# Kernel optimization log

Hardware: AMD Instinct MI355X
Metric: run time of the kernel (lower is better)

The kernel has to match this reference:

```python
import jax, jax.numpy as jnp
import numpy as np
import math

EPS = 1e-5  # BatchNorm eps

def _bn(x, g, b):
    # eval-mode BatchNorm2d with fresh running stats (mean=0, var=1); x is NCHW
    s = g / jnp.sqrt(1.0 + EPS)
    return x * s[None, :, None, None] + b[None, :, None, None]

def _conv1x1(x, w, b):
    # x: (B,C,H,W), w: (O,C)
    return jnp.einsum('bchw,oc->bohw', x, w) + b[None, :, None, None]

def _selective_scan(xs, dts, A, Bs, Cs, D, delta_bias):
    # xs,dts: (B,K,D,L); A: (K,D,N); Bs,Cs: (B,K,N,L); D,delta_bias: (K,D)
    delta = jax.nn.softplus(dts + delta_bias[None, :, :, None])  # (B,K,D,L)
    d_t = jnp.moveaxis(delta, -1, 0)  # (L,B,K,D)
    u_t = jnp.moveaxis(xs, -1, 0)     # (L,B,K,D)
    B_t = jnp.moveaxis(Bs, -1, 0)     # (L,B,K,N)
    C_t = jnp.moveaxis(Cs, -1, 0)     # (L,B,K,N)

    def step(h, inp):
        d, u, b, c = inp
        dA = jnp.exp(d[..., None] * A)                       # (B,K,D,N)
        h = dA * h + (d * u)[..., None] * b[:, :, None, :]   # (B,K,D,N)
        y = jnp.einsum('bkdn,bkn->bkd', h, c)
        return h, y

    h0 = jnp.zeros(xs.shape[:3] + (A.shape[-1],), xs.dtype)
    _, ys = jax.lax.scan(step, h0, (d_t, u_t, B_t, C_t))
    y = jnp.moveaxis(ys, 0, -1)  # (B,K,D,L)
    return y + D[None, :, :, None] * xs

def _ssm(x, x_proj_w, dt_w, dt_b, A_logs, Ds):
    # x: (B,C,H,W); 4-directional VMamba SS2D core
    B, C, H, W = x.shape
    L = H * W
    K = 4
    N = A_logs.shape[-1]
    R = dt_w.shape[-1]
    x_hw = x.reshape(B, C, L)
    x_wh = jnp.transpose(x, (0, 1, 3, 2)).reshape(B, C, L)
    xs = jnp.stack([x_hw, x_wh, x_hw[..., ::-1], x_wh[..., ::-1]], axis=1)  # (B,K,C,L)
    x_dbl = jnp.einsum('bkdl,kcd->bkcl', xs, x_proj_w)
    dts = jnp.einsum('bkrl,kdr->bkdl', x_dbl[:, :, :R], dt_w)
    Bs = x_dbl[:, :, R:R + N]
    Cs = x_dbl[:, :, R + N:R + 2 * N]
    A = -jnp.exp(A_logs).reshape(K, C, N)
    out_y = _selective_scan(xs, dts, A, Bs, Cs, Ds.reshape(K, C), dt_b)  # (B,K,C,L)
    inv = out_y[:, 2:4, :, ::-1]

    def wh_to_hw(t):
        return jnp.transpose(t.reshape(B, C, W, H), (0, 1, 3, 2)).reshape(B, C, L)

    y = out_y[:, 0] + inv[:, 0] + wh_to_hw(out_y[:, 1]) + wh_to_hw(inv[:, 1])
    return jnp.transpose(y, (0, 2, 1))  # (B,L,C)

def _forward(x, qkv_w, proj_w, proj_b, dw_w, dw_b, bn1_g, bn1_b,
             ci_w1, ci_b1, ci_bn_g, ci_bn_b, ci_w2, ci_b2,
             si_w1, si_b1, si_bn_g, si_bn_b, si_w2, si_b2,
             x_proj_w, dt_w, dt_b, A_logs, Ds, H, W):
    B, L, C = x.shape
    v = x @ qkv_w.T                                           # (B,L,C)
    v_img = jnp.transpose(v, (0, 2, 1)).reshape(B, C, H, W)
    # SSM (attention-replacement) branch
    att = _ssm(v_img, x_proj_w, dt_w, dt_b, A_logs, Ds)       # (B,L,C)
    # depthwise conv branch
    conv_x = jax.lax.conv_general_dilated(
        v_img, dw_w, (1, 1), 'SAME', feature_group_count=C,
        dimension_numbers=('NCHW', 'OIHW', 'NCHW'))
    conv_x = jax.nn.gelu(_bn(conv_x + dw_b[None, :, None, None], bn1_g, bn1_b), approximate=False)
    # C-Map: channel interaction from conv branch
    pooled = jnp.mean(conv_x, axis=(2, 3), keepdims=True)     # (B,C,1,1)
    cm = jax.nn.gelu(_bn(_conv1x1(pooled, ci_w1, ci_b1), ci_bn_g, ci_bn_b), approximate=False)
    cm = _conv1x1(cm, ci_w2, ci_b2)                           # (B,C,1,1)
    channel_map = cm.reshape(B, 1, C)
    # S-Map: spatial interaction from ssm branch
    att_img = jnp.transpose(att, (0, 2, 1)).reshape(B, C, H, W)
    sm = jax.nn.gelu(_bn(_conv1x1(att_img, si_w1, si_b1), si_bn_g, si_bn_b), approximate=False)
    sm = _conv1x1(sm, si_w2, si_b2)                           # (B,1,H,W)
    # adaptive interaction
    att = att * jax.nn.sigmoid(channel_map)
    conv_x = jax.nn.sigmoid(sm) * conv_x
    conv_x = jnp.transpose(conv_x.reshape(B, C, L), (0, 2, 1))
    return (att + conv_x) @ proj_w.T + proj_b

def setup_inputs() -> dict:
    key = jax.random.key(0)
    ks = jax.random.split(key, 16)
    Bsz, H, W, C = 2, 64, 64, 96
    N, K = 16, 4
    R = math.ceil(C / 16)  # dt_rank = 6
    L = H * W
    rn = lambda k, s, sc: jax.random.normal(k, s, jnp.float32) * sc
    inp = {
        'x': rn(ks[0], (Bsz, L, C), 1.0),
        'H': H, 'W': W,
        'qkv_w': rn(ks[1], (C, C), C ** -0.5),
        'proj_w': rn(ks[2], (C, C), C ** -0.5),
        'proj_b': jnp.zeros((C,), jnp.float32),
        'dw_w': rn(ks[3], (C, 1, 3, 3), 0.2),
        'dw_b': jnp.zeros((C,), jnp.float32),
        'bn1_g': jnp.ones((C,), jnp.float32), 'bn1_b': jnp.zeros((C,), jnp.float32),
        'ci_w1': rn(ks[4], (C // 8, C), C ** -0.5), 'ci_b1': jnp.zeros((C // 8,), jnp.float32),
        'ci_bn_g': jnp.ones((C // 8,), jnp.float32), 'ci_bn_b': jnp.zeros((C // 8,), jnp.float32),
        'ci_w2': rn(ks[5], (C, C // 8), (C // 8) ** -0.5), 'ci_b2': jnp.zeros((C,), jnp.float32),
        'si_w1': rn(ks[6], (C // 16, C), C ** -0.5), 'si_b1': jnp.zeros((C // 16,), jnp.float32),
        'si_bn_g': jnp.ones((C // 16,), jnp.float32), 'si_bn_b': jnp.zeros((C // 16,), jnp.float32),
        'si_w2': rn(ks[7], (1, C // 16), (C // 16) ** -0.5), 'si_b2': jnp.zeros((1,), jnp.float32),
        'x_proj_w': rn(ks[8], (K, R + 2 * N, C), C ** -0.5),
        'dt_w': jax.random.uniform(ks[9], (K, C, R), jnp.float32, -(R ** -0.5), R ** -0.5),
    }
    dt = jnp.exp(jax.random.uniform(ks[10], (K, C)) * (math.log(0.1) - math.log(0.001)) + math.log(0.001))
    dt = jnp.clip(dt, 1e-4, None)
    inp['dt_b'] = dt + jnp.log(-jnp.expm1(-dt))  # inverse-softplus init
    inp['A_logs'] = jnp.log(jnp.tile(jnp.arange(1, N + 1, dtype=jnp.float32), (K * C, 1)))  # (K*C, N)
    inp['Ds'] = jnp.ones((K * C,), jnp.float32)
    return inp

def reference(x, H, W, qkv_w, proj_w, proj_b, dw_w, dw_b, bn1_g, bn1_b,
              ci_w1, ci_b1, ci_bn_g, ci_bn_b, ci_w2, ci_b2,
              si_w1, si_b1, si_bn_g, si_bn_b, si_w2, si_b2,
              x_proj_w, dt_w, dt_b, A_logs, Ds):
    return _forward(x, qkv_w, proj_w, proj_b, dw_w, dw_b, bn1_g, bn1_b,
                    ci_w1, ci_b1, ci_bn_g, ci_bn_b, ci_w2, ci_b2,
                    si_w1, si_b1, si_bn_g, si_bn_b, si_w2, si_b2,
                    x_proj_w, dt_w, dt_b, A_logs, Ds, H, W)
```

## Files before the change

kernel.cpp:

```cpp
#include <hip/hip_runtime.h>
#include <math.h>

#define BB 2
#define CC 96
#define LL 4096
#define KK 4
#define SS 128
#define CHL 32
#define XD 40
#define BNS 0.9999950000374997f

__device__ __forceinline__ float fsigmoid(float x){ return 1.f/(1.f+__expf(-x)); }
__device__ __forceinline__ float fgelu(float x){ return 0.5f*x*(1.f+erff(x*0.70710678118654752f)); }
__device__ __forceinline__ void pow_tree(float q, float* Q){
  float q2=q*q, q4=q2*q2, q8=q4*q4;
  Q[0]=q;      Q[1]=q2;     Q[2]=q2*q;   Q[3]=q4;
  Q[4]=q4*q;   Q[5]=q4*q2;  Q[6]=Q[5]*q; Q[7]=q8;
  Q[8]=q8*q;   Q[9]=q8*q2;  Q[10]=Q[9]*q;Q[11]=q8*q4;
  Q[12]=Q[11]*q; Q[13]=Q[11]*q2; Q[14]=Q[13]*q; Q[15]=q8*q8;
}

__global__ __launch_bounds__(512) void kQ(const float* __restrict__ x,
                                          const float* __restrict__ qkv_w,
                                          float* __restrict__ v_hw){
  __shared__ float xl[96*33];
  int bid = blockIdx.x;
  int b = bid >> 7;
  int l0 = (bid & 127) << 5;
  int tid = threadIdx.x;
  for (int idx = tid; idx < 32*96; idx += 512){
    int pos = idx/96, c = idx - pos*96;
    xl[c*33+pos] = x[((size_t)b*LL + l0 + pos)*CC + c];
  }
  __syncthreads();
  int wv = tid >> 6, lane = tid & 63, pos = lane & 31, ch = lane >> 5;
  int c0 = ch*48;
  int ob = __builtin_amdgcn_readfirstlane(wv*12);
  float acc[12];
#pragma unroll
  for (int j = 0; j < 12; ++j) acc[j] = 0.f;
  for (int i = 0; i < 48; ++i){
    int c = c0 + i;
    float xv = xl[c*33+pos];
#pragma unroll
    for (int j = 0; j < 12; ++j) acc[j] += xv * qkv_w[(ob+j)*96 + c];
  }
#pragma unroll
  for (int j = 0; j < 12; ++j) acc[j] += __shfl_xor(acc[j], 32);
  if (ch == 0){
#pragma unroll
    for (int j = 0; j < 12; ++j)
      v_hw[((size_t)b*CC + ob + j)*LL + l0 + pos] = acc[j];
  }
}

__global__ __launch_bounds__(256) void kT(const float* __restrict__ src,
                                          float* __restrict__ dst){
  __shared__ float t[64*65];
  int bid = blockIdx.x;
  size_t base = (size_t)bid * LL;
  int tid = threadIdx.x;
  for (int idx = tid; idx < 4096; idx += 256){
    int h = idx>>6, w = idx&63;
    t[w*65+h] = src[base+idx];
  }
  __syncthreads();
  for (int idx = tid; idx < 4096; idx += 256)
    dst[base+idx] = t[(idx>>6)*65 + (idx&63)];
}

__global__ __launch_bounds__(512) void kP(const float* __restrict__ v_hw,
                                          const float* __restrict__ v_wh,
                                          const float* __restrict__ xpw,
                                          float* __restrict__ xdbl){
  __shared__ float ul[96*33];
  __shared__ float ol[32*40];
  int bid = blockIdx.x;
  int tile = bid & 127; int bk = bid >> 7; int k = bk & 3; int b = bk >> 2;
  int l0 = tile << 5;
  int tid = threadIdx.x;
  const float* vs = (k & 1) ? v_wh : v_hw;
  bool fwd = (k < 2);
  for (int idx = tid; idx < 96*32; idx += 512){
    int c = idx >> 5, t = idx & 31;
    int srci = fwd ? (l0+t) : (LL-1-(l0+t));
    ul[c*33+t] = vs[((size_t)b*CC + c)*LL + srci];
  }
  if (tid < 32){ ol[tid*40+6] = 0.f; ol[tid*40+7] = 0.f; }
  __syncthreads();
  int wv = tid >> 6, lane = tid & 63, pos = lane & 31, ch = lane >> 5;
  int c0 = ch*48;
  int obase = __builtin_amdgcn_readfirstlane((wv < 6) ? wv*5 : 30 + (wv-6)*4);
  int ocnt  = (wv < 6) ? 5 : 4;
  const float* wk = xpw + k*38*96;
  float acc[5];
#pragma unroll
  for (int j = 0; j < 5; ++j) acc[j] = 0.f;
  for (int i = 0; i < 48; ++i){
    int c = c0 + i;
    float uv = ul[c*33+pos];
#pragma unroll
    for (int j = 0; j < 5; ++j)
      if (j < ocnt) acc[j] += uv * wk[(obase+j)*96 + c];
  }
#pragma unroll
  for (int j = 0; j < 5; ++j) acc[j] += __shfl_xor(acc[j], 32);
  if (ch == 0){
#pragma unroll
    for (int j = 0; j < 5; ++j){
      if (j < ocnt){
        int cc = obase + j;
        int off = (cc < 6) ? cc : cc+2;
        ol[pos*40 + off] = acc[j];
      }
    }
  }
  __syncthreads();
  size_t rec = (((size_t)b*KK + k)*LL + l0)*XD;
  for (int idx = tid; idx < 32*40; idx += 512)
    xdbl[rec + idx] = ol[idx];
}

__global__ __launch_bounds__(128) void kC(const float* __restrict__ v_hw,
                                          const float* __restrict__ v_wh,
                                          const float* __restrict__ xdbl,
                                          const float* __restrict__ dt_w,
                                          const float* __restrict__ dt_b,
                                          const float* __restrict__ dw_w,
                                          const float* __restrict__ dw_b,
                                          const float* __restrict__ bn_g,
                                          const float* __restrict__ bn_b,
                                          float* __restrict__ hend,
                                          float* __restrict__ Pbuf,
                                          float* __restrict__ convx,
                                          float* __restrict__ partial2){
  __shared__ float ul[96*33];
  __shared__ __align__(16) float xl[CHL*XD];
  __shared__ float pl[34*65];
  __shared__ float red[2];
  int tid = threadIdx.x;
  if (blockIdx.x < 1024){
    int bid = blockIdx.x;
    int s = bid & 127; int bk = bid >> 7; int k = bk & 3; int b = bk >> 2;
    const float* vs = (k & 1) ? v_wh : v_hw;
    bool fwd = (k < 2);
    size_t xbase = (((size_t)b*KK + k)*LL + s*CHL)*XD;
    const float4* xg = (const float4*)(xdbl + xbase);
    float4* xl4 = (float4*)xl;
    for (int idx = tid; idx < CHL*XD/4; idx += 128) xl4[idx] = xg[idx];
    for (int idx = tid; idx < 96*CHL; idx += 128){
      int cr = idx >> 5, t = idx & 31;
      int gt = s*CHL + t;
      int srci = fwd ? gt : (LL-1-gt);
      ul[cr*33+t] = vs[((size_t)b*CC + cr)*LL + srci];
    }
    int c = tid;
    float dtw[6], dtb = 0.f, h[16], sumd = 0.f;
    if (c < 96){
      int cb = k*96+c;
#pragma unroll
      for (int r = 0; r < 6; ++r) dtw[r] = dt_w[cb*6+r];
      dtb = dt_b[cb];
#pragma unroll
      for (int n = 0; n < 16; ++n) h[n] = 0.f;
    }
    __syncthreads();
    if (c < 96){
      for (int t = 0; t < CHL; ++t){
        const float* xr = xl + t*XD;
        float4 r03 = *(const float4*)xr;
        float2 r45 = *(const float2*)(xr+4);
        float draw = dtb + r03.x*dtw[0]+r03.y*dtw[1]+r03.z*dtw[2]
                         + r03.w*dtw[3]+r45.x*dtw[4]+r45.y*dtw[5];
        float e = __expf(draw);
        float delta = (draw > 20.f) ? draw : __logf(1.f+e);
        float qd = __builtin_amdgcn_rcpf(1.f+e);
        sumd += delta;
        float du = delta * ul[c*33+t];
        float4 b0 = *(const float4*)(xr+8),  b1 = *(const float4*)(xr+12),
               b2 = *(const float4*)(xr+16), b3 = *(const float4*)(xr+20);
        float Bv[16] = {b0.x,b0.y,b0.z,b0.w, b1.x,b1.y,b1.z,b1.w,
                        b2.x,b2.y,b2.z,b2.w, b3.x,b3.y,b3.z,b3.w};
        float Q[16]; pow_tree(qd, Q);
#pragma unroll
        for (int n = 0; n < 16; ++n) h[n] = h[n]*Q[n] + du*Bv[n];
      }
      float P[16]; pow_tree(__expf(-sumd), P);
      size_t obf = ((((size_t)b*KK+k)*SS + s)*96 + c)*16;
#pragma unroll
      for (int q = 0; q < 4; ++q){
        *(float4*)(hend + obf + q*4) = make_float4(h[q*4+0],h[q*4+1],h[q*4+2],h[q*4+3]);
        *(float4*)(Pbuf + obf + q*4) = make_float4(P[q*4+0],P[q*4+1],P[q*4+2],P[q*4+3]);
      }
    }
  } else {
    int cb = blockIdx.x - 1024;
    int plane = cb >> 1;
    int half = cb & 1;
    int c = plane % 96;
    int h0 = half*32;
    size_t base = (size_t)plane * LL;
    for (int idx = tid; idx < 34*64; idx += 128){
      int r = idx >> 6, w = idx & 63;
      int h = h0 - 1 + r;
      pl[r*65+w] = (h >= 0 && h < 64) ? v_hw[base + h*64 + w] : 0.f;
    }
    __syncthreads();
    float w9[9];
#pragma unroll
    for (int i = 0; i < 9; ++i) w9[i] = dw_w[c*9+i];
    float bias = dw_b[c], g = bn_g[c]*BNS, bb = bn_b[c];
    float lsum = 0.f;
    for (int idx = tid; idx < 2048; idx += 128){
      int hh = idx >> 6, w = idx & 63;
      float acc = bias;
#pragma unroll
      for (int i = 0; i < 3; ++i)
#pragma unroll
        for (int j = -1; j <= 1; ++j){
          int w2 = w + j;
          if (w2 >= 0 && w2 < 64) acc += pl[(hh+i)*65 + w2] * w9[i*3 + (j+1)];
        }
      float val = fgelu(acc*g + bb);
      convx[base + (h0+hh)*64 + w] = val;
      lsum += val;
    }
#pragma unroll
    for (int off = 32; off >= 1; off >>= 1) lsum += __shfl_down(lsum, off);
    if ((tid & 63) == 0) red[tid>>6] = lsum;
    __syncthreads();
    if (tid == 0) partial2[cb] = red[0] + red[1];
  }
}

__global__ __launch_bounds__(256) void kD(const float* __restrict__ hend,
                                          const float* __restrict__ Pbuf,
                                          float* __restrict__ Hin){
  int bid = blockIdx.x;
  int cpair = bid % 48; int bk = bid / 48;
  int tid = threadIdx.x;
  int sg = tid & 7;
  int n  = (tid >> 3) & 15;
  int c  = cpair*2 + (tid >> 7);
  int lane = tid & 63;
  size_t base = (size_t)bk*SS*1536 + c*16 + n;
  float he[16], pb[16];
  float A = 1.f, Bv = 0.f;
#pragma unroll
  for (int i = 0; i < 16; ++i){
    size_t off = base + (size_t)(sg*16+i)*1536;
    he[i] = hend[off]; pb[i] = Pbuf[off];
    A *= pb[i];
    Bv = he[i] + pb[i]*Bv;
  }
#pragma unroll
  for (int d = 1; d <= 4; d <<= 1){
    float Ap = __shfl(A, lane-d);
    float Bp = __shfl(Bv, lane-d);
    if (sg >= d){ Bv = A*Bp + Bv; A = A*Ap; }
  }
  float Bin = __shfl(Bv, lane-1);
  float hacc = (sg == 0) ? 0.f : Bin;
#pragma unroll
  for (int i = 0; i < 16; ++i){
    size_t off = base + (size_t)(sg*16+i)*1536;
    Hin[off] = hacc;
    hacc = he[i] + pb[i]*hacc;
  }
}

__global__ __launch_bounds__(128) void kE(const float* __restrict__ v_hw,
                                          const float* __restrict__ v_wh,
                                          const float* __restrict__ xdbl,
                                          const float* __restrict__ dt_w,
                                          const float* __restrict__ dt_b,
                                          const float* __restrict__ Hin,
                                          float* __restrict__ ybuf){
  __shared__ float ul[96*33];
  __shared__ float yl[96*33];
  __shared__ __align__(16) float xl[CHL*XD];
  int bid = blockIdx.x;
  int s = bid & 127; int bk = bid >> 7; int k = bk & 3; int b = bk >> 2;
  int tid = threadIdx.x;
  const float* vs = (k & 1) ? v_wh : v_hw;
  bool fwd = (k < 2);
  float* yo = ybuf + (size_t)k*786432;
  size_t xbase = (((size_t)b*KK + k)*LL + s*CHL)*XD;
  const float4* xg = (const float4*)(xdbl + xbase);
  float4* xl4 = (float4*)xl;
  for (int idx = tid; idx < CHL*XD/4; idx += 128) xl4[idx] = xg[idx];
  for (int idx = tid; idx < 96*CHL; idx += 128){
    int cr = idx >> 5, t = idx & 31;
    int gt = s*CHL + t;
    int srci = fwd ? gt : (LL-1-gt);
    ul[cr*33+t] = vs[((size_t)b*CC + cr)*LL + srci];
  }
  int c = tid;
  float dtw[6], dtb = 0.f, h[16];
  if (c < 96){
    int cb = k*96 + c;
#pragma unroll
    for (int r = 0; r < 6; ++r) dtw[r] = dt_w[cb*6+r];
    dtb = dt_b[cb];
    size_t hb = ((((size_t)b*KK+k)*SS + s)*96 + c)*16;
#pragma unroll
    for (int q = 0; q < 4; ++q){
      float4 hv = *(const float4*)(Hin + hb + q*4);
      h[q*4+0]=hv.x; h[q*4+1]=hv.y; h[q*4+2]=hv.z; h[q*4+3]=hv.w;
    }
  }
  __syncthreads();
  if (c < 96){
    for (int t = 0; t < CHL; ++t){
      const float* xr = xl + t*XD;
      float4 r03 = *(const float4*)xr;
      float2 r45 = *(const float2*)(xr+4);
      float draw = dtb + r03.x*dtw[0]+r03.y*dtw[1]+r03.z*dtw[2]
                       + r03.w*dtw[3]+r45.x*dtw[4]+r45.y*dtw[5];
      float e = __expf(draw);
      float delta = (draw > 20.f) ? draw : __logf(1.f+e);
      float qd = __builtin_amdgcn_rcpf(1.f+e);
      float du = delta * ul[c*33+t];
      float4 b0 = *(const float4*)(xr+8),  b1 = *(const float4*)(xr+12),
             b2 = *(const float4*)(xr+16), b3 = *(const float4*)(xr+20);
      float4 c0v = *(const float4*)(xr+24), c1v = *(const float4*)(xr+28),
             c2v = *(const float4*)(xr+32), c3v = *(const float4*)(xr+36);
      float Bv[16] = {b0.x,b0.y,b0.z,b0.w, b1.x,b1.y,b1.z,b1.w,
                      b2.x,b2.y,b2.z,b2.w, b3.x,b3.y,b3.z,b3.w};
      float Cv[16] = {c0v.x,c0v.y,c0v.z,c0v.w, c1v.x,c1v.y,c1v.z,c1v.w,
                      c2v.x,c2v.y,c2v.z,c2v.w, c3v.x,c3v.y,c3v.z,c3v.w};
      float Q[16]; pow_tree(qd, Q);
      float ya[4] = {0.f,0.f,0.f,0.f};
#pragma unroll
      for (int n = 0; n < 16; ++n){
        h[n] = h[n]*Q[n] + du*Bv[n];
        ya[n & 3] += h[n]*Cv[n];
      }
      yl[c*33+t] = (ya[0]+ya[1]) + (ya[2]+ya[3]);
    }
  }
  __syncthreads();
  for (int idx = tid; idx < 96*CHL; idx += 128){
    int cr = idx >> 5, t = idx & 31;
    int gt = s*CHL + t;
    int pos = fwd ? gt : (LL-1-gt);
    yo[((size_t)b*CC + cr)*LL + pos] = yl[cr*33+t];
  }
}

__global__ __launch_bounds__(256) void kF(const float* __restrict__ ybuf,
                                          const float* __restrict__ v_hw,
                                          const float* __restrict__ Ds,
                                          float* __restrict__ att){
  __shared__ float t1[64*65];
  int bid = blockIdx.x; int c = bid % 96;
  size_t base = (size_t)bid * LL;
  int tid = threadIdx.x;
  const float* yk0 = ybuf;
  const float* yk1 = ybuf + 786432;
  const float* yk2 = ybuf + 2*786432;
  const float* yk3 = ybuf + 3*786432;
  for (int idx = tid; idx < 4096; idx += 256)
    t1[(idx & 63)*65 + (idx >> 6)] = yk1[base+idx] + yk3[base+idx];
  __syncthreads();
  float dsum = Ds[c] + Ds[96+c] + Ds[192+c] + Ds[288+c];
  for (int idx = tid; idx < 4096; idx += 256){
    int h = idx >> 6, w = idx & 63;
    att[base+idx] = yk0[base+idx] + yk2[base+idx] + t1[h*65+w] + dsum*v_hw[base+idx];
  }
}

__global__ __launch_bounds__(512) void kG(const float* __restrict__ att,
                                          const float* __restrict__ convx,
                                          const float* __restrict__ partial2,
                                          const float* __restrict__ ci_w1, const float* __restrict__ ci_b1,
                                          const float* __restrict__ ci_g1, const float* __restrict__ ci_bb1,
                                          const float* __restrict__ ci_w2, const float* __restrict__ ci_b2,
                                          const float* __restrict__ si_w1, const float* __restrict__ si_b1,
                                          const float* __restrict__ si_g1, const float* __restrict__ si_bb1,
                                          const float* __restrict__ si_w2, const float* __restrict__ si_b2,
                                          const float* __restrict__ proj_w,
                                          const float* __restrict__ proj_b,
                                          float* __restrict__ out){
  __shared__ float ga[96*33];
  __shared__ float gc[96*33];
  __shared__ float pool[96];
  __shared__ float mid[12];
  __shared__ float smj[6*33];
  __shared__ float smv[32];
  __shared__ float cmv[96];
  int bid = blockIdx.x;
  int b = bid >> 7; int l0 = (bid & 127) << 5;
  int tid = threadIdx.x;
  for (int idx = tid; idx < 96*32; idx += 512){
    int c = idx >> 5, t = idx & 31;
    size_t gsrc = ((size_t)b*CC + c)*LL + l0 + t;
    ga[c*33+t] = att[gsrc];
    gc[c*33+t] = convx[gsrc];
  }
  if (tid < 96) pool[tid] = (partial2[(b*96+tid)*2] + partial2[(b*96+tid)*2+1]) * (1.f/4096.f);
  __syncthreads();
  int wv = tid >> 6, lane = tid & 63, pos = lane & 31, ch = lane >> 5;
  if (wv < 6){
    int j = __builtin_amdgcn_readfirstlane(wv);
    float dot = 0.f;
    for (int i = 0; i < 48; ++i){
      int c = ch*48 + i;
      dot += ga[c*33+pos] * si_w1[j*96+c];
    }
    dot += __shfl_xor(dot, 32);
    if (ch == 0)
      smj[j*33+pos] = si_w2[j]*fgelu((dot+si_b1[j])*si_g1[j]*BNS + si_bb1[j]);
  } else if (wv == 6 && lane < 12){
    int j2 = lane;
    float a = ci_b1[j2];
    for (int c = 0; c < 96; ++c) a += ci_w1[j2*96+c]*pool[c];
    mid[j2] = fgelu(a*ci_g1[j2]*BNS + ci_bb1[j2]);
  }
  __syncthreads();
  if (tid < 32){
    float sv = si_b2[0];
#pragma unroll
    for (int j = 0; j < 6; ++j) sv += smj[j*33+tid];
    smv[tid] = fsigmoid(sv);
  }
  if (tid >= 64 && tid < 160){
    int c = tid - 64;
    float a = ci_b2[c];
#pragma unroll
    for (int j = 0; j < 12; ++j) a += ci_w2[c*12+j]*mid[j];
    cmv[c] = fsigmoid(a);
  }
  __syncthreads();
  for (int idx = tid; idx < 96*32; idx += 512){
    int c = idx >> 5, t = idx & 31;
    ga[c*33+t] = ga[c*33+t]*cmv[c] + gc[c*33+t]*smv[t];
  }
  __syncthreads();
  int ob = __builtin_amdgcn_readfirstlane(wv*12);
  float acc[12];
#pragma unroll
  for (int j = 0; j < 12; ++j) acc[j] = 0.f;
  for (int i = 0; i < 48; ++i){
    int c = ch*48 + i;
    float gv = ga[c*33+pos];
#pragma unroll
    for (int j = 0; j < 12; ++j) acc[j] += gv * proj_w[(ob+j)*96 + c];
  }
#pragma unroll
  for (int j = 0; j < 12; ++j) acc[j] += __shfl_xor(acc[j], 32);
  if (ch == 0){
    float* ol = gc;
#pragma unroll
    for (int j = 0; j < 12; ++j) ol[pos*97 + ob + j] = acc[j] + proj_b[ob+j];
  }
  __syncthreads();
  const float* ol = gc;
  for (int idx = tid; idx < 32*96; idx += 512){
    int p = idx/96, o = idx - p*96;
    out[((size_t)b*LL + l0 + p)*CC + o] = ol[p*97+o];
  }
}

extern "C" void kernel_launch(void* const* d_in, const int* in_sizes, int n_in,
                              void* d_out, int out_size, void* d_ws, size_t ws_size,
                              hipStream_t stream) {
  const float* x      = (const float*)d_in[0];
  const float* qkv_w  = (const float*)d_in[3];
  const float* proj_w = (const float*)d_in[4];
  const float* proj_b = (const float*)d_in[5];
  const float* dw_w   = (const float*)d_in[6];
  const float* dw_b   = (const float*)d_in[7];
  const float* bn1_g  = (const float*)d_in[8];
  const float* bn1_b  = (const float*)d_in[9];
  const float* ci_w1  = (const float*)d_in[10];
  const float* ci_b1  = (const float*)d_in[11];
  const float* ci_bn_g= (const float*)d_in[12];
  const float* ci_bn_b= (const float*)d_in[13];
  const float* ci_w2  = (const float*)d_in[14];
  const float* ci_b2  = (const float*)d_in[15];
  const float* si_w1  = (const float*)d_in[16];
  const float* si_b1  = (const float*)d_in[17];
  const float* si_bn_g= (const float*)d_in[18];
  const float* si_bn_b= (const float*)d_in[19];
  const float* si_w2  = (const float*)d_in[20];
  const float* si_b2  = (const float*)d_in[21];
  const float* xpw    = (const float*)d_in[22];
  const float* dt_w   = (const float*)d_in[23];
  const float* dt_b   = (const float*)d_in[24];
  const float* Ds     = (const float*)d_in[26];

  float* ws    = (float*)d_ws;
  float* v_hw  = ws;
  float* v_wh  = v_hw + 786432;
  float* xdbl  = v_wh + 786432;
  float* hend  = xdbl + 1310720;
  float* Pbuf  = hend + 1572864;
  float* Hin   = Pbuf + 1572864;
  float* convx = Hin  + 1572864;
  float* partial2 = convx + 786432;
  float* ybuf  = hend;
  float* att   = xdbl;
  float* out = (float*)d_out;

  hipLaunchKernelGGL(kQ, dim3(256),  dim3(512), 0, stream, x, qkv_w, v_hw);
  hipLaunchKernelGGL(kT, dim3(192),  dim3(256), 0, stream, v_hw, v_wh);
  hipLaunchKernelGGL(kP, dim3(1024), dim3(512), 0, stream, v_hw, v_wh, xpw, xdbl);
  hipLaunchKernelGGL(kC, dim3(1408), dim3(128), 0, stream, v_hw, v_wh, xdbl, dt_w, dt_b,
                     dw_w, dw_b, bn1_g, bn1_b, hend, Pbuf, convx, partial2);
  hipLaunchKernelGGL(kD, dim3(384),  dim3(256), 0, stream, hend, Pbuf, Hin);
  hipLaunchKernelGGL(kE, dim3(1024), dim3(128), 0, stream, v_hw, v_wh, xdbl, dt_w, dt_b, Hin, ybuf);
  hipLaunchKernelGGL(kF, dim3(192),  dim3(256), 0, stream, ybuf, v_hw, Ds, att);
  hipLaunchKernelGGL(kG, dim3(256),  dim3(512), 0, stream, att, convx, partial2,
                     ci_w1, ci_b1, ci_bn_g, ci_bn_b, ci_w2, ci_b2,
                     si_w1, si_b1, si_bn_g, si_bn_b, si_w2, si_b2,
                     proj_w, proj_b, out);
}
```

Baseline: 217.5 us.

## Fuse all stages into one persistent cooperative kernel with grid syncs

Replaces the eight separate kernel launches with a single cooperative persistent kernel that runs each stage as a grid-strided phase separated by grid-wide syncs. A fallback path launches the phases as separate kernels. It also changes data layouts: qkv output is written both channel-last and planar, the transpose becomes a row copy in channel-last order, and the scans read u directly from global memory with a prefetch instead of staging it in shared memory. The aim is to remove launch gaps and tail effects between stages, at the cost of grid-sync overhead, a grid capped at 512 blocks, and lower occupancy from the shared-memory union.

```diff
diff --git a/kernel.cpp b/kernel.cpp
--- a/kernel.cpp
+++ b/kernel.cpp
@@ -1,5 +1,8 @@
 #include <hip/hip_runtime.h>
+#include <hip/hip_cooperative_groups.h>
 #include <math.h>
+
+namespace cg = cooperative_groups;
 
 #define BB 2
 #define CC 96
@@ -20,152 +23,186 @@
   Q[12]=Q[11]*q; Q[13]=Q[11]*q2; Q[14]=Q[13]*q; Q[15]=q8*q8;
 }
 
-__global__ __launch_bounds__(512) void kQ(const float* __restrict__ x,
-                                          const float* __restrict__ qkv_w,
-                                          float* __restrict__ v_hw){
-  __shared__ float xl[96*33];
-  int bid = blockIdx.x;
-  int b = bid >> 7;
-  int l0 = (bid & 127) << 5;
+struct Params {
+  const float *x,*qkv_w,*proj_w,*proj_b,*dw_w,*dw_b,*bn_g,*bn_b;
+  const float *ci_w1,*ci_b1,*ci_g1,*ci_bb1,*ci_w2,*ci_b2;
+  const float *si_w1,*si_b1,*si_g1,*si_bb1,*si_w2,*si_b2;
+  const float *xpw,*dt_w,*dt_b,*Ds;
+  float *vT_hw,*vP_hw,*vT_wh,*xdbl,*hend,*Pbuf,*Hin,*convxP,*partial,*ybuf,*out;
+};
+
+struct Ph1 { float xl[96*33]; };
+struct Ph2 { float t[64*65]; float red[4]; };
+struct Ph3 { float ul[96*33]; float ol[32*40]; };
+struct Ph4 { float xl[2][CHL*XD]; };
+struct Ph8 { float ga[96*33]; float gcv[96*33]; float pool[96]; float dsc[96];
+             float mid[12]; float smj[6*33]; float smv[32]; float cmv[96]; };
+union __align__(16) SMem { Ph1 p1; Ph2 p2; Ph3 p3; Ph4 p4; Ph8 p8; };
+
+__device__ void ph_qkv(SMem* sm, const Params& p){
+  int tid = threadIdx.x, wv = tid>>6, lane = tid&63;
+  int G = gridDim.x;
+  for (int it = blockIdx.x; it < 256; it += G){
+    int b = it >> 7, l0 = (it & 127) << 5;
+    __syncthreads();
+    const float* xs = p.x + ((size_t)b*LL + l0)*CC;
+    for (int idx = tid; idx < 3072; idx += 256){
+      int t = idx/96, c = idx - t*96;
+      sm->p1.xl[c*33+t] = xs[idx];
+    }
+    __syncthreads();
+    int pos = lane & 31, ch = lane >> 5, c0 = ch*48;
+    int ob = __builtin_amdgcn_readfirstlane(wv*24);
+    float acc[24];
+#pragma unroll
+    for (int j = 0; j < 24; ++j) acc[j] = 0.f;
+    for (int i = 0; i < 48; ++i){
+      int c = c0 + i;
+      float xv = sm->p1.xl[c*33+pos];
+#pragma unroll
+      for (int j = 0; j < 24; ++j) acc[j] += xv * p.qkv_w[(ob+j)*CC + c];
+    }
+#pragma unroll
+    for (int j = 0; j < 24; ++j) acc[j] += __shfl_xor(acc[j], 32);
+    if (ch == 0){
+      size_t rT = ((size_t)b*LL + l0 + pos)*CC + ob;
+#pragma unroll
+      for (int j = 0; j < 24; ++j) p.vT_hw[rT + j] = acc[j];
+#pragma unroll
+      for (int j = 0; j < 24; ++j)
+        p.vP_hw[((size_t)b*CC + ob + j)*LL + l0 + pos] = acc[j];
+    }
+  }
+}
+
+__device__ void ph_convcopy(SMem* sm, const Params& p){
+  int tid = threadIdx.x, wv = tid>>6;
+  int G = gridDim.x;
+  for (int it = blockIdx.x; it < 448; it += G){
+    __syncthreads();
+    if (it < 192){
+      int c = it % 96;
+      size_t base = (size_t)it * LL;
+      for (int idx = tid; idx < 4096; idx += 256)
+        sm->p2.t[(idx>>6)*65 + (idx&63)] = p.vP_hw[base+idx];
+      __syncthreads();
+      float w9[9];
+#pragma unroll
+      for (int i = 0; i < 9; ++i) w9[i] = p.dw_w[c*9+i];
+      float bias = p.dw_b[c], g = p.bn_g[c]*BNS, bb = p.bn_b[c];
+      float lsum = 0.f;
+      for (int idx = tid; idx < 4096; idx += 256){
+        int h = idx>>6, w = idx&63;
+        float acc = bias;
+#pragma unroll
+        for (int i = -1; i <= 1; ++i)
+#pragma unroll
+          for (int j = -1; j <= 1; ++j){
+            int hh = h+i, w2 = w+j;
+            if (hh>=0 && hh<64 && w2>=0 && w2<64) acc += sm->p2.t[hh*65+w2]*w9[(i+1)*3+(j+1)];
+          }
+        float val = fgelu(acc*g + bb);
+        p.convxP[base+idx] = val;
+        lsum += val;
+      }
+#pragma unroll
+      for (int off = 32; off >= 1; off >>= 1) lsum += __shfl_down(lsum, off);
+      if ((tid & 63) == 0) sm->p2.red[wv] = lsum;
+      __syncthreads();
+      if (tid == 0) p.partial[it] = sm->p2.red[0]+sm->p2.red[1]+sm->p2.red[2]+sm->p2.red[3];
+    } else {
+      int ci = it - 192;
+      int b = ci >> 7; int p0 = (ci & 127) << 5;
+      int w = p0 >> 6; int h0 = p0 & 63;
+      for (int idx4 = tid; idx4 < 768; idx4 += 256){
+        int r = idx4/24, c4 = idx4 - r*24;
+        float4 v = *(const float4*)(p.vT_hw + ((size_t)b*LL + (h0+r)*64 + w)*CC + c4*4);
+        *(float4*)(p.vT_wh + ((size_t)b*LL + p0 + r)*CC + c4*4) = v;
+      }
+    }
+  }
+}
+
+__device__ void ph_proj(SMem* sm, const Params& p){
+  int tid = threadIdx.x, wv = tid>>6, lane = tid&63;
+  int G = gridDim.x;
+  for (int it = blockIdx.x; it < 1024; it += G){
+    int tile = it & 127, bk = it >> 7, k = bk & 3, b = bk >> 2;
+    int l0 = tile << 5;
+    const float* uT = (k & 1) ? p.vT_wh : p.vT_hw;
+    bool fwd = (k < 2);
+    __syncthreads();
+    for (int idx = tid; idx < 3072; idx += 256){
+      int t = idx/96, c = idx - t*96;
+      int srci = fwd ? (l0+t) : (LL-1-(l0+t));
+      sm->p3.ul[c*33+t] = uT[((size_t)b*LL + srci)*CC + c];
+    }
+    if (tid < 32){ sm->p3.ol[tid*40+6] = 0.f; sm->p3.ol[tid*40+7] = 0.f; }
+    __syncthreads();
+    int pos = lane & 31, ch = lane >> 5, c0 = ch*48;
+    int rw0 = __builtin_amdgcn_readfirstlane(wv*10);
+    int rcnt = (wv < 3) ? 10 : 8;
+    const float* wk = p.xpw + k*38*96;
+    float acc[10];
+#pragma unroll
+    for (int j = 0; j < 10; ++j) acc[j] = 0.f;
+    for (int i = 0; i < 48; ++i){
+      int c = c0 + i;
+      float uv = sm->p3.ul[c*33+pos];
+#pragma unroll
+      for (int j = 0; j < 10; ++j)
+        if (j < rcnt) acc[j] += uv * wk[(rw0+j)*96 + c];
+    }
+#pragma unroll
+    for (int j = 0; j < 10; ++j) acc[j] += __shfl_xor(acc[j], 32);
+    if (ch == 0){
+#pragma unroll
+      for (int j = 0; j < 10; ++j){
+        if (j < rcnt){
+          int cc = rw0 + j;
+          int off = (cc < 6) ? cc : cc+2;
+          sm->p3.ol[pos*40 + off] = acc[j];
+        }
+      }
+    }
+    __syncthreads();
+    size_t rec = (((size_t)b*KK + k)*LL + l0)*XD;
+    for (int idx = tid; idx < 1280; idx += 256)
+      p.xdbl[rec + idx] = sm->p3.ol[idx];
+  }
+}
+
+__device__ void ph_scan1(SMem* sm, const Params& p){
   int tid = threadIdx.x;
-  for (int idx = tid; idx < 32*96; idx += 512){
-    int pos = idx/96, c = idx - pos*96;
-    xl[c*33+pos] = x[((size_t)b*LL + l0 + pos)*CC + c];
-  }
-  __syncthreads();
-  int wv = tid >> 6, lane = tid & 63, pos = lane & 31, ch = lane >> 5;
-  int c0 = ch*48;
-  int ob = __builtin_amdgcn_readfirstlane(wv*12);
-  float acc[12];
-#pragma unroll
-  for (int j = 0; j < 12; ++j) acc[j] = 0.f;
-  for (int i = 0; i < 48; ++i){
-    int c = c0 + i;
-    float xv = xl[c*33+pos];
-#pragma unroll
-    for (int j = 0; j < 12; ++j) acc[j] += xv * qkv_w[(ob+j)*96 + c];
-  }
-#pragma unroll
-  for (int j = 0; j < 12; ++j) acc[j] += __shfl_xor(acc[j], 32);
-  if (ch == 0){
-#pragma unroll
-    for (int j = 0; j < 12; ++j)
-      v_hw[((size_t)b*CC + ob + j)*LL + l0 + pos] = acc[j];
-  }
-}
-
-__global__ __launch_bounds__(256) void kT(const float* __restrict__ src,
-                                          float* __restrict__ dst){
-  __shared__ float t[64*65];
-  int bid = blockIdx.x;
-  size_t base = (size_t)bid * LL;
-  int tid = threadIdx.x;
-  for (int idx = tid; idx < 4096; idx += 256){
-    int h = idx>>6, w = idx&63;
-    t[w*65+h] = src[base+idx];
-  }
-  __syncthreads();
-  for (int idx = tid; idx < 4096; idx += 256)
-    dst[base+idx] = t[(idx>>6)*65 + (idx&63)];
-}
-
-__global__ __launch_bounds__(512) void kP(const float* __restrict__ v_hw,
-                                          const float* __restrict__ v_wh,
-                                          const float* __restrict__ xpw,
-                                          float* __restrict__ xdbl){
-  __shared__ float ul[96*33];
-  __shared__ float ol[32*40];
-  int bid = blockIdx.x;
-  int tile = bid & 127; int bk = bid >> 7; int k = bk & 3; int b = bk >> 2;
-  int l0 = tile << 5;
-  int tid = threadIdx.x;
-  const float* vs = (k & 1) ? v_wh : v_hw;
-  bool fwd = (k < 2);
-  for (int idx = tid; idx < 96*32; idx += 512){
-    int c = idx >> 5, t = idx & 31;
-    int srci = fwd ? (l0+t) : (LL-1-(l0+t));
-    ul[c*33+t] = vs[((size_t)b*CC + c)*LL + srci];
-  }
-  if (tid < 32){ ol[tid*40+6] = 0.f; ol[tid*40+7] = 0.f; }
-  __syncthreads();
-  int wv = tid >> 6, lane = tid & 63, pos = lane & 31, ch = lane >> 5;
-  int c0 = ch*48;
-  int obase = __builtin_amdgcn_readfirstlane((wv < 6) ? wv*5 : 30 + (wv-6)*4);
-  int ocnt  = (wv < 6) ? 5 : 4;
-  const float* wk = xpw + k*38*96;
-  float acc[5];
-#pragma unroll
-  for (int j = 0; j < 5; ++j) acc[j] = 0.f;
-  for (int i = 0; i < 48; ++i){
-    int c = c0 + i;
-    float uv = ul[c*33+pos];
-#pragma unroll
-    for (int j = 0; j < 5; ++j)
-      if (j < ocnt) acc[j] += uv * wk[(obase+j)*96 + c];
-  }
-#pragma unroll
-  for (int j = 0; j < 5; ++j) acc[j] += __shfl_xor(acc[j], 32);
-  if (ch == 0){
-#pragma unroll
-    for (int j = 0; j < 5; ++j){
-      if (j < ocnt){
-        int cc = obase + j;
-        int off = (cc < 6) ? cc : cc+2;
-        ol[pos*40 + off] = acc[j];
-      }
-    }
-  }
-  __syncthreads();
-  size_t rec = (((size_t)b*KK + k)*LL + l0)*XD;
-  for (int idx = tid; idx < 32*40; idx += 512)
-    xdbl[rec + idx] = ol[idx];
-}
-
-__global__ __launch_bounds__(128) void kC(const float* __restrict__ v_hw,
-                                          const float* __restrict__ v_wh,
-                                          const float* __restrict__ xdbl,
-                                          const float* __restrict__ dt_w,
-                                          const float* __restrict__ dt_b,
-                                          const float* __restrict__ dw_w,
-                                          const float* __restrict__ dw_b,
-                                          const float* __restrict__ bn_g,
-                                          const float* __restrict__ bn_b,
-                                          float* __restrict__ hend,
-                                          float* __restrict__ Pbuf,
-                                          float* __restrict__ convx,
-                                          float* __restrict__ partial2){
-  __shared__ float ul[96*33];
-  __shared__ __align__(16) float xl[CHL*XD];
-  __shared__ float pl[34*65];
-  __shared__ float red[2];
-  int tid = threadIdx.x;
-  if (blockIdx.x < 1024){
-    int bid = blockIdx.x;
-    int s = bid & 127; int bk = bid >> 7; int k = bk & 3; int b = bk >> 2;
-    const float* vs = (k & 1) ? v_wh : v_hw;
+  int G = gridDim.x;
+  int sub = tid >> 7, stid = tid & 127;
+  for (int base = blockIdx.x*2; base < 1024; base += G*2){
+    int it = base + sub;
+    int s = it & 127, bk = it >> 7, k = bk & 3, b = bk >> 2;
+    const float* uT = (k & 1) ? p.vT_wh : p.vT_hw;
     bool fwd = (k < 2);
-    size_t xbase = (((size_t)b*KK + k)*LL + s*CHL)*XD;
-    const float4* xg = (const float4*)(xdbl + xbase);
-    float4* xl4 = (float4*)xl;
-    for (int idx = tid; idx < CHL*XD/4; idx += 128) xl4[idx] = xg[idx];
-    for (int idx = tid; idx < 96*CHL; idx += 128){
-      int cr = idx >> 5, t = idx & 31;
-      int gt = s*CHL + t;
-      int srci = fwd ? gt : (LL-1-gt);
-      ul[cr*33+t] = vs[((size_t)b*CC + cr)*LL + srci];
-    }
-    int c = tid;
-    float dtw[6], dtb = 0.f, h[16], sumd = 0.f;
+    __syncthreads();
+    const float4* xg = (const float4*)(p.xdbl + (((size_t)b*KK + k)*LL + s*CHL)*XD);
+    float4* xl4 = (float4*)sm->p4.xl[sub];
+    for (int i = stid; i < 320; i += 128) xl4[i] = xg[i];
+    __syncthreads();
+    int c = stid;
     if (c < 96){
       int cb = k*96+c;
-#pragma unroll
-      for (int r = 0; r < 6; ++r) dtw[r] = dt_w[cb*6+r];
-      dtb = dt_b[cb];
+      float dtw[6];
+#pragma unroll
+      for (int r = 0; r < 6; ++r) dtw[r] = p.dt_w[cb*6+r];
+      float dtb = p.dt_b[cb];
+      float h[16];
 #pragma unroll
       for (int n = 0; n < 16; ++n) h[n] = 0.f;
-    }
-    __syncthreads();
-    if (c < 96){
+      float sumd = 0.f;
+      int r0 = fwd ? s*CHL : (LL-1 - s*CHL);
+      int rs = fwd ? CC : -CC;
+      const float* up = uT + ((size_t)b*LL + r0)*CC + c;
+      float u0 = up[0];
+      float u1 = up[rs];
+      const float* xl = sm->p4.xl[sub];
       for (int t = 0; t < CHL; ++t){
         const float* xr = xl + t*XD;
         float4 r03 = *(const float4*)xr;
@@ -176,7 +213,10 @@
         float delta = (draw > 20.f) ? draw : __logf(1.f+e);
         float qd = __builtin_amdgcn_rcpf(1.f+e);
         sumd += delta;
-        float du = delta * ul[c*33+t];
+        float du = delta * u0;
+        u0 = u1;
+        int noff = (t+2 < CHL) ? (t+2)*rs : 0;
+        u1 = up[noff];
         float4 b0 = *(const float4*)(xr+8),  b1 = *(const float4*)(xr+12),
                b2 = *(const float4*)(xr+16), b3 = *(const float4*)(xr+20);
         float Bv[16] = {b0.x,b0.y,b0.z,b0.w, b1.x,b1.y,b1.z,b1.w,
@@ -189,330 +229,293 @@
       size_t obf = ((((size_t)b*KK+k)*SS + s)*96 + c)*16;
 #pragma unroll
       for (int q = 0; q < 4; ++q){
-        *(float4*)(hend + obf + q*4) = make_float4(h[q*4+0],h[q*4+1],h[q*4+2],h[q*4+3]);
-        *(float4*)(Pbuf + obf + q*4) = make_float4(P[q*4+0],P[q*4+1],P[q*4+2],P[q*4+3]);
-      }
-    }
-  } else {
-    int cb = blockIdx.x - 1024;
-    int plane = cb >> 1;
-    int half = cb & 1;
-    int c = plane % 96;
-    int h0 = half*32;
-    size_t base = (size_t)plane * LL;
-    for (int idx = tid; idx < 34*64; idx += 128){
-      int r = idx >> 6, w = idx & 63;
-      int h = h0 - 1 + r;
-      pl[r*65+w] = (h >= 0 && h < 64) ? v_hw[base + h*64 + w] : 0.f;
-    }
-    __syncthreads();
-    float w9[9];
-#pragma unroll
-    for (int i = 0; i < 9; ++i) w9[i] = dw_w[c*9+i];
-    float bias = dw_b[c], g = bn_g[c]*BNS, bb = bn_b[c];
-    float lsum = 0.f;
-    for (int idx = tid; idx < 2048; idx += 128){
-      int hh = idx >> 6, w = idx & 63;
-      float acc = bias;
-#pragma unroll
-      for (int i = 0; i < 3; ++i)
-#pragma unroll
-        for (int j = -1; j <= 1; ++j){
-          int w2 = w + j;
-          if (w2 >= 0 && w2 < 64) acc += pl[(hh+i)*65 + w2] * w9[i*3 + (j+1)];
+        *(float4*)(p.hend + obf + q*4) = make_float4(h[q*4+0],h[q*4+1],h[q*4+2],h[q*4+3]);
+        *(float4*)(p.Pbuf + obf + q*4) = make_float4(P[q*4+0],P[q*4+1],P[q*4+2],P[q*4+3]);
+      }
+    }
+  }
+}
+
+__device__ void ph_scan2(const Params& p){
+  int tid = threadIdx.x, lane = tid & 63;
+  int G = gridDim.x;
+  for (int it = blockIdx.x; it < 384; it += G){
+    int cpair = it % 48, bk = it / 48;
+    int sg = tid & 7;
+    int n  = (tid >> 3) & 15;
+    int c  = cpair*2 + (tid >> 7);
+    size_t base = (size_t)bk*SS*1536 + c*16 + n;
+    float he[16], pb[16];
+    float A = 1.f, Bv = 0.f;
+#pragma unroll
+    for (int i = 0; i < 16; ++i){
+      size_t off = base + (size_t)(sg*16+i)*1536;
+      he[i] = p.hend[off]; pb[i] = p.Pbuf[off];
+      A *= pb[i];
+      Bv = he[i] + pb[i]*Bv;
+    }
+#pragma unroll
+    for (int d = 1; d <= 4; d <<= 1){
+      float Ap = __shfl(A, lane-d);
+      float Bp = __shfl(Bv, lane-d);
+      if (sg >= d){ Bv = A*Bp + Bv; A = A*Ap; }
+    }
+    float Bin = __shfl(Bv, lane-1);
+    float hacc = (sg == 0) ? 0.f : Bin;
+#pragma unroll
+    for (int i = 0; i < 16; ++i){
+      size_t off = base + (size_t)(sg*16+i)*1536;
+      p.Hin[off] = hacc;
+      hacc = he[i] + pb[i]*hacc;
+    }
+  }
+}
+
+__device__ void ph_scan3(SMem* sm, const Params& p){
+  int tid = threadIdx.x;
+  int G = gridDim.x;
+  int sub = tid >> 7, stid = tid & 127;
+  for (int base = blockIdx.x*2; base < 1024; base += G*2){
+    int it = base + sub;
+    int s = it & 127, bk = it >> 7, k = bk & 3, b = bk >> 2;
+    const float* uT = (k & 1) ? p.vT_wh : p.vT_hw;
+    bool fwd = (k < 2);
+    float* yo = p.ybuf + (size_t)k*786432;
+    __syncthreads();
+    const float4* xg = (const float4*)(p.xdbl + (((size_t)b*KK + k)*LL + s*CHL)*XD);
+    float4* xl4 = (float4*)sm->p4.xl[sub];
+    for (int i = stid; i < 320; i += 128) xl4[i] = xg[i];
+    __syncthreads();
+    int c = stid;
+    if (c < 96){
+      int cb = k*96+c;
+      float dtw[6];
+#pragma unroll
+      for (int r = 0; r < 6; ++r) dtw[r] = p.dt_w[cb*6+r];
+      float dtb = p.dt_b[cb];
+      float h[16];
+      size_t hb = ((((size_t)b*KK+k)*SS + s)*96 + c)*16;
+#pragma unroll
+      for (int q = 0; q < 4; ++q){
+        float4 hv = *(const float4*)(p.Hin + hb + q*4);
+        h[q*4+0]=hv.x; h[q*4+1]=hv.y; h[q*4+2]=hv.z; h[q*4+3]=hv.w;
+      }
+      int r0 = fwd ? s*CHL : (LL-1 - s*CHL);
+      int rs = fwd ? CC : -CC;
+      const float* up = uT + ((size_t)b*LL + r0)*CC + c;
+      float* yp = yo + ((size_t)b*LL + r0)*CC + c;
+      float u0 = up[0];
+      float u1 = up[rs];
+      const float* xl = sm->p4.xl[sub];
+      for (int t = 0; t < CHL; ++t){
+        const float* xr = xl + t*XD;
+        float4 r03 = *(const float4*)xr;
+        float2 r45 = *(const float2*)(xr+4);
+        float draw = dtb + r03.x*dtw[0]+r03.y*dtw[1]+r03.z*dtw[2]
+                         + r03.w*dtw[3]+r45.x*dtw[4]+r45.y*dtw[5];
+        float e = __expf(draw);
+        float delta = (draw > 20.f) ? draw : __logf(1.f+e);
+        float qd = __builtin_amdgcn_rcpf(1.f+e);
+        float du = delta * u0;
+        u0 = u1;
+        int noff = (t+2 < CHL) ? (t+2)*rs : 0;
+        u1 = up[noff];
+        float4 b0 = *(const float4*)(xr+8),  b1 = *(const float4*)(xr+12),
+               b2 = *(const float4*)(xr+16), b3 = *(const float4*)(xr+20);
+        float4 c0v = *(const float4*)(xr+24), c1v = *(const float4*)(xr+28),
+               c2v = *(const float4*)(xr+32), c3v = *(const float4*)(xr+36);
+        float Bv[16] = {b0.x,b0.y,b0.z,b0.w, b1.x,b1.y,b1.z,b1.w,
+                        b2.x,b2.y,b2.z,b2.w, b3.x,b3.y,b3.z,b3.w};
+        float Cv[16] = {c0v.x,c0v.y,c0v.z,c0v.w, c1v.x,c1v.y,c1v.z,c1v.w,
+                        c2v.x,c2v.y,c2v.z,c2v.w, c3v.x,c3v.y,c3v.z,c3v.w};
+        float Q[16]; pow_tree(qd, Q);
+        float ya[4] = {0.f,0.f,0.f,0.f};
+#pragma unroll
+        for (int n = 0; n < 16; ++n){
+          h[n] = h[n]*Q[n] + du*Bv[n];
+          ya[n & 3] += h[n]*Cv[n];
         }
-      float val = fgelu(acc*g + bb);
-      convx[base + (h0+hh)*64 + w] = val;
-      lsum += val;
-    }
-#pragma unroll
-    for (int off = 32; off >= 1; off >>= 1) lsum += __shfl_down(lsum, off);
-    if ((tid & 63) == 0) red[tid>>6] = lsum;
-    __syncthreads();
-    if (tid == 0) partial2[cb] = red[0] + red[1];
-  }
-}
-
-__global__ __launch_bounds__(256) void kD(const float* __restrict__ hend,
-                                          const float* __restrict__ Pbuf,
-                                          float* __restrict__ Hin){
-  int bid = blockIdx.x;
-  int cpair = bid % 48; int bk = bid / 48;
-  int tid = threadIdx.x;
-  int sg = tid & 7;
-  int n  = (tid >> 3) & 15;
-  int c  = cpair*2 + (tid >> 7);
-  int lane = tid & 63;
-  size_t base = (size_t)bk*SS*1536 + c*16 + n;
-  float he[16], pb[16];
-  float A = 1.f, Bv = 0.f;
-#pragma unroll
-  for (int i = 0; i < 16; ++i){
-    size_t off = base + (size_t)(sg*16+i)*1536;
-    he[i] = hend[off]; pb[i] = Pbuf[off];
-    A *= pb[i];
-    Bv = he[i] + pb[i]*Bv;
-  }
-#pragma unroll
-  for (int d = 1; d <= 4; d <<= 1){
-    float Ap = __shfl(A, lane-d);
-    float Bp = __shfl(Bv, lane-d);
-    if (sg >= d){ Bv = A*Bp + Bv; A = A*Ap; }
-  }
-  float Bin = __shfl(Bv, lane-1);
-  float hacc = (sg == 0) ? 0.f : Bin;
-#pragma unroll
-  for (int i = 0; i < 16; ++i){
-    size_t off = base + (size_t)(sg*16+i)*1536;
-    Hin[off] = hacc;
-    hacc = he[i] + pb[i]*hacc;
-  }
-}
-
-__global__ __launch_bounds__(128) void kE(const float* __restrict__ v_hw,
-                                          const float* __restrict__ v_wh,
-                                          const float* __restrict__ xdbl,
-                                          const float* __restrict__ dt_w,
-                                          const float* __restrict__ dt_b,
-                                          const float* __restrict__ Hin,
-                                          float* __restrict__ ybuf){
-  __shared__ float ul[96*33];
-  __shared__ float yl[96*33];
-  __shared__ __align__(16) float xl[CHL*XD];
-  int bid = blockIdx.x;
-  int s = bid & 127; int bk = bid >> 7; int k = bk & 3; int b = bk >> 2;
-  int tid = threadIdx.x;
-  const float* vs = (k & 1) ? v_wh : v_hw;
-  bool fwd = (k < 2);
-  float* yo = ybuf + (size_t)k*786432;
-  size_t xbase = (((size_t)b*KK + k)*LL + s*CHL)*XD;
-  const float4* xg = (const float4*)(xdbl + xbase);
-  float4* xl4 = (float4*)xl;
-  for (int idx = tid; idx < CHL*XD/4; idx += 128) xl4[idx] = xg[idx];
-  for (int idx = tid; idx < 96*CHL; idx += 128){
-    int cr = idx >> 5, t = idx & 31;
-    int gt = s*CHL + t;
-    int srci = fwd ? gt : (LL-1-gt);
-    ul[cr*33+t] = vs[((size_t)b*CC + cr)*LL + srci];
-  }
-  int c = tid;
-  float dtw[6], dtb = 0.f, h[16];
-  if (c < 96){
-    int cb = k*96 + c;
-#pragma unroll
-    for (int r = 0; r < 6; ++r) dtw[r] = dt_w[cb*6+r];
-    dtb = dt_b[cb];
-    size_t hb = ((((size_t)b*KK+k)*SS + s)*96 + c)*16;
-#pragma unroll
-    for (int q = 0; q < 4; ++q){
-      float4 hv = *(const float4*)(Hin + hb + q*4);
-      h[q*4+0]=hv.x; h[q*4+1]=hv.y; h[q*4+2]=hv.z; h[q*4+3]=hv.w;
-    }
-  }
-  __syncthreads();
-  if (c < 96){
-    for (int t = 0; t < CHL; ++t){
-      const float* xr = xl + t*XD;
-      float4 r03 = *(const float4*)xr;
-      float2 r45 = *(const float2*)(xr+4);
-      float draw = dtb + r03.x*dtw[0]+r03.y*dtw[1]+r03.z*dtw[2]
-                       + r03.w*dtw[3]+r45.x*dtw[4]+r45.y*dtw[5];
-      float e = __expf(draw);
-      float delta = (draw > 20.f) ? draw : __logf(1.f+e);
-      float qd = __builtin_amdgcn_rcpf(1.f+e);
-      float du = delta * ul[c*33+t];
-      float4 b0 = *(const float4*)(xr+8),  b1 = *(const float4*)(xr+12),
-             b2 = *(const float4*)(xr+16), b3 = *(const float4*)(xr+20);
-      float4 c0v = *(const float4*)(xr+24), c1v = *(const float4*)(xr+28),
-             c2v = *(const float4*)(xr+32), c3v = *(const float4*)(xr+36);
-      float Bv[16] = {b0.x,b0.y,b0.z,b0.w, b1.x,b1.y,b1.z,b1.w,
-                      b2.x,b2.y,b2.z,b2.w, b3.x,b3.y,b3.z,b3.w};
-      float Cv[16] = {c0v.x,c0v.y,c0v.z,c0v.w, c1v.x,c1v.y,c1v.z,c1v.w,
-                      c2v.x,c2v.y,c2v.z,c2v.w, c3v.x,c3v.y,c3v.z,c3v.w};
-      float Q[16]; pow_tree(qd, Q);
-      float ya[4] = {0.f,0.f,0.f,0.f};
-#pragma unroll
-      for (int n = 0; n < 16; ++n){
-        h[n] = h[n]*Q[n] + du*Bv[n];
-        ya[n & 3] += h[n]*Cv[n];
-      }
-      yl[c*33+t] = (ya[0]+ya[1]) + (ya[2]+ya[3]);
-    }
-  }
-  __syncthreads();
-  for (int idx = tid; idx < 96*CHL; idx += 128){
-    int cr = idx >> 5, t = idx & 31;
-    int gt = s*CHL + t;
-    int pos = fwd ? gt : (LL-1-gt);
-    yo[((size_t)b*CC + cr)*LL + pos] = yl[cr*33+t];
-  }
-}
-
-__global__ __launch_bounds__(256) void kF(const float* __restrict__ ybuf,
-                                          const float* __restrict__ v_hw,
-                                          const float* __restrict__ Ds,
-                                          float* __restrict__ att){
-  __shared__ float t1[64*65];
-  int bid = blockIdx.x; int c = bid % 96;
-  size_t base = (size_t)bid * LL;
-  int tid = threadIdx.x;
-  const float* yk0 = ybuf;
-  const float* yk1 = ybuf + 786432;
-  const float* yk2 = ybuf + 2*786432;
-  const float* yk3 = ybuf + 3*786432;
-  for (int idx = tid; idx < 4096; idx += 256)
-    t1[(idx & 63)*65 + (idx >> 6)] = yk1[base+idx] + yk3[base+idx];
-  __syncthreads();
-  float dsum = Ds[c] + Ds[96+c] + Ds[192+c] + Ds[288+c];
-  for (int idx = tid; idx < 4096; idx += 256){
-    int h = idx >> 6, w = idx & 63;
-    att[base+idx] = yk0[base+idx] + yk2[base+idx] + t1[h*65+w] + dsum*v_hw[base+idx];
-  }
-}
-
-__global__ __launch_bounds__(512) void kG(const float* __restrict__ att,
-                                          const float* __restrict__ convx,
-                                          const float* __restrict__ partial2,
-                                          const float* __restrict__ ci_w1, const float* __restrict__ ci_b1,
-                                          const float* __restrict__ ci_g1, const float* __restrict__ ci_bb1,
-                                          const float* __restrict__ ci_w2, const float* __restrict__ ci_b2,
-                                          const float* __restrict__ si_w1, const float* __restrict__ si_b1,
-                                          const float* __restrict__ si_g1, const float* __restrict__ si_bb1,
-                                          const float* __restrict__ si_w2, const float* __restrict__ si_b2,
-                                          const float* __restrict__ proj_w,
-                                          const float* __restrict__ proj_b,
-                                          float* __restrict__ out){
-  __shared__ float ga[96*33];
-  __shared__ float gc[96*33];
-  __shared__ float pool[96];
-  __shared__ float mid[12];
-  __shared__ float smj[6*33];
-  __shared__ float smv[32];
-  __shared__ float cmv[96];
-  int bid = blockIdx.x;
-  int b = bid >> 7; int l0 = (bid & 127) << 5;
-  int tid = threadIdx.x;
-  for (int idx = tid; idx < 96*32; idx += 512){
-    int c = idx >> 5, t = idx & 31;
-    size_t gsrc = ((size_t)b*CC + c)*LL + l0 + t;
-    ga[c*33+t] = att[gsrc];
-    gc[c*33+t] = convx[gsrc];
-  }
-  if (tid < 96) pool[tid] = (partial2[(b*96+tid)*2] + partial2[(b*96+tid)*2+1]) * (1.f/4096.f);
-  __syncthreads();
-  int wv = tid >> 6, lane = tid & 63, pos = lane & 31, ch = lane >> 5;
-  if (wv < 6){
-    int j = __builtin_amdgcn_readfirstlane(wv);
-    float dot = 0.f;
+        yp[t*rs] = (ya[0]+ya[1]) + (ya[2]+ya[3]);
+      }
+    }
+  }
+}
+
+__device__ void ph_gate(SMem* sm, const Params& p){
+  int tid = threadIdx.x, wv = tid>>6, lane = tid&63;
+  int G = gridDim.x;
+  const float* y0 = p.ybuf;
+  const float* y1 = p.ybuf + 786432;
+  const float* y2 = p.ybuf + 2*786432;
+  const float* y3 = p.ybuf + 3*786432;
+  for (int it = blockIdx.x; it < 256; it += G){
+    int b = it >> 7, l0 = (it & 127) << 5;
+    int hh = l0 >> 6, w0 = l0 & 63;
+    __syncthreads();
+    if (tid < 96){
+      sm->p8.dsc[tid] = p.Ds[tid]+p.Ds[96+tid]+p.Ds[192+tid]+p.Ds[288+tid];
+      sm->p8.pool[tid] = p.partial[b*96+tid] * (1.f/4096.f);
+    }
+    __syncthreads();
+    for (int idx = tid; idx < 3072; idx += 256){
+      int t = idx/96, c = idx - t*96;
+      size_t rhw = ((size_t)b*LL + l0 + t)*CC + c;
+      size_t rwh = ((size_t)b*LL + ((w0+t)<<6) + hh)*CC + c;
+      sm->p8.ga[c*33+t] = y0[rhw] + y2[rhw] + y1[rwh] + y3[rwh] + sm->p8.dsc[c]*p.vT_hw[rhw];
+    }
+    for (int idx = tid; idx < 3072; idx += 256){
+      int c = idx >> 5, t = idx & 31;
+      sm->p8.gcv[c*33+t] = p.convxP[((size_t)b*CC + c)*LL + l0 + t];
+    }
+    __syncthreads();
+    int pos = lane & 31, ch = lane >> 5;
+    if (wv < 3){
+      int j0 = __builtin_amdgcn_readfirstlane(2*wv);
+      float d0 = 0.f, d1 = 0.f;
+      for (int i = 0; i < 48; ++i){
+        int c = ch*48 + i;
+        float g = sm->p8.ga[c*33+pos];
+        d0 += g * p.si_w1[j0*96+c];
+        d1 += g * p.si_w1[(j0+1)*96+c];
+      }
+      d0 += __shfl_xor(d0, 32);
+      d1 += __shfl_xor(d1, 32);
+      if (ch == 0){
+        sm->p8.smj[j0*33+pos]     = p.si_w2[j0]  *fgelu((d0+p.si_b1[j0])  *p.si_g1[j0]  *BNS + p.si_bb1[j0]);
+        sm->p8.smj[(j0+1)*33+pos] = p.si_w2[j0+1]*fgelu((d1+p.si_b1[j0+1])*p.si_g1[j0+1]*BNS + p.si_bb1[j0+1]);
+      }
+    } else if (lane < 12){
+      int j2 = lane;
+      float a = p.ci_b1[j2];
+      for (int c = 0; c < 96; ++c) a += p.ci_w1[j2*96+c]*sm->p8.pool[c];
+      sm->p8.mid[j2] = fgelu(a*p.ci_g1[j2]*BNS + p.ci_bb1[j2]);
+    }
+    __syncthreads();
+    if (tid < 32){
+      float sv = p.si_b2[0];
+#pragma unroll
+      for (int j = 0; j < 6; ++j) sv += sm->p8.smj[j*33+tid];
+      sm->p8.smv[tid] = fsigmoid(sv);
+    }
+    if (tid >= 64 && tid < 160){
+      int c = tid - 64;
+      float a = p.ci_b2[c];
+#pragma unroll
+      for (int j = 0; j < 12; ++j) a += p.ci_w2[c*12+j]*sm->p8.mid[j];
+      sm->p8.cmv[c] = fsigmoid(a);
+    }
+    __syncthreads();
+    for (int idx = tid; idx < 3072; idx += 256){
+      int c = idx >> 5, t = idx & 31;
+      sm->p8.ga[c*33+t] = sm->p8.ga[c*33+t]*sm->p8.cmv[c] + sm->p8.gcv[c*33+t]*sm->p8.smv[t];
+    }
+    __syncthreads();
+    int ob = __builtin_amdgcn_readfirstlane(wv*24);
+    int c0 = ch*48;
+    float acc[24];
+#pragma unroll
+    for (int j = 0; j < 24; ++j) acc[j] = 0.f;
     for (int i = 0; i < 48; ++i){
-      int c = ch*48 + i;
-      dot += ga[c*33+pos] * si_w1[j*96+c];
-    }
-    dot += __shfl_xor(dot, 32);
-    if (ch == 0)
-      smj[j*33+pos] = si_w2[j]*fgelu((dot+si_b1[j])*si_g1[j]*BNS + si_bb1[j]);
-  } else if (wv == 6 && lane < 12){
-    int j2 = lane;
-    float a = ci_b1[j2];
-    for (int c = 0; c < 96; ++c) a += ci_w1[j2*96+c]*pool[c];
-    mid[j2] = fgelu(a*ci_g1[j2]*BNS + ci_bb1[j2]);
-  }
-  __syncthreads();
-  if (tid < 32){
-    float sv = si_b2[0];
-#pragma unroll
-    for (int j = 0; j < 6; ++j) sv += smj[j*33+tid];
-    smv[tid] = fsigmoid(sv);
-  }
-  if (tid >= 64 && tid < 160){
-    int c = tid - 64;
-    float a = ci_b2[c];
-#pragma unroll
-    for (int j = 0; j < 12; ++j) a += ci_w2[c*12+j]*mid[j];
-    cmv[c] = fsigmoid(a);
-  }
-  __syncthreads();
-  for (int idx = tid; idx < 96*32; idx += 512){
-    int c = idx >> 5, t = idx & 31;
-    ga[c*33+t] = ga[c*33+t]*cmv[c] + gc[c*33+t]*smv[t];
-  }
-  __syncthreads();
-  int ob = __builtin_amdgcn_readfirstlane(wv*12);
-  float acc[12];
-#pragma unroll
-  for (int j = 0; j < 12; ++j) acc[j] = 0.f;
-  for (int i = 0; i < 48; ++i){
-    int c = ch*48 + i;
-    float gv = ga[c*33+pos];
-#pragma unroll
-    for (int j = 0; j < 12; ++j) acc[j] += gv * proj_w[(ob+j)*96 + c];
-  }
-#pragma unroll
-  for (int j = 0; j < 12; ++j) acc[j] += __shfl_xor(acc[j], 32);
-  if (ch == 0){
-    float* ol = gc;
-#pragma unroll
-    for (int j = 0; j < 12; ++j) ol[pos*97 + ob + j] = acc[j] + proj_b[ob+j];
-  }
-  __syncthreads();
-  const float* ol = gc;
-  for (int idx = tid; idx < 32*96; idx += 512){
-    int p = idx/96, o = idx - p*96;
-    out[((size_t)b*LL + l0 + p)*CC + o] = ol[p*97+o];
-  }
-}
+      int c = c0 + i;
+      float gv = sm->p8.ga[c*33+pos];
+#pragma unroll
+      for (int j = 0; j < 24; ++j) acc[j] += gv * p.proj_w[(ob+j)*96 + c];
+    }
+#pragma unroll
+    for (int j = 0; j < 24; ++j) acc[j] += __shfl_xor(acc[j], 32);
+    __syncthreads();
+    float* ol = sm->p8.gcv;
+    if (ch == 0){
+#pragma unroll
+      for (int j = 0; j < 24; ++j) ol[pos*97 + ob + j] = acc[j] + p.proj_b[ob+j];
+    }
+    __syncthreads();
+    float* os = p.out + ((size_t)b*LL + l0)*CC;
+    for (int idx = tid; idx < 3072; idx += 256){
+      int pp = idx/96, o = idx - pp*96;
+      os[idx] = ol[pp*97+o];
+    }
+  }
+}
+
+__global__ __launch_bounds__(256, 2) void mega(Params p){
+  cg::grid_group gg = cg::this_grid();
+  __shared__ SMem sm;
+  ph_qkv(&sm, p);       __threadfence(); gg.sync();
+  ph_convcopy(&sm, p);  __threadfence(); gg.sync();
+  ph_proj(&sm, p);      __threadfence(); gg.sync();
+  ph_scan1(&sm, p);     __threadfence(); gg.sync();
+  ph_scan2(p);          __threadfence(); gg.sync();
+  ph_scan3(&sm, p);     __threadfence(); gg.sync();
+  ph_gate(&sm, p);
+}
+
+__global__ __launch_bounds__(256,2) void kP1(Params p){ __shared__ SMem sm; ph_qkv(&sm, p); }
+__global__ __launch_bounds__(256,2) void kP2(Params p){ __shared__ SMem sm; ph_convcopy(&sm, p); }
+__global__ __launch_bounds__(256,2) void kP3(Params p){ __shared__ SMem sm; ph_proj(&sm, p); }
+__global__ __launch_bounds__(256,2) void kP4(Params p){ __shared__ SMem sm; ph_scan1(&sm, p); }
+__global__ __launch_bounds__(256,2) void kP5(Params p){ ph_scan2(p); }
+__global__ __launch_bounds__(256,2) void kP6(Params p){ __shared__ SMem sm; ph_scan3(&sm, p); }
+__global__ __launch_bounds__(256,2) void kP7(Params p){ __shared__ SMem sm; ph_gate(&sm, p); }
 
 extern "C" void kernel_launch(void* const* d_in, const int* in_sizes, int n_in,
                               void* d_out, int out_size, void* d_ws, size_t ws_size,
                               hipStream_t stream) {
-  const float* x      = (const float*)d_in[0];
-  const float* qkv_w  = (const float*)d_in[3];
-  const float* proj_w = (const float*)d_in[4];
-  const float* proj_b = (const float*)d_in[5];
-  const float* dw_w   = (const float*)d_in[6];
-  const float* dw_b   = (const float*)d_in[7];
-  const float* bn1_g  = (const float*)d_in[8];
-  const float* bn1_b  = (const float*)d_in[9];
-  const float* ci_w1  = (const float*)d_in[10];
-  const float* ci_b1  = (const float*)d_in[11];
-  const float* ci_bn_g= (const float*)d_in[12];
-  const float* ci_bn_b= (const float*)d_in[13];
-  const float* ci_w2  = (const float*)d_in[14];
-  const float* ci_b2  = (const float*)d_in[15];
-  const float* si_w1  = (const float*)d_in[16];
-  const float* si_b1  = (const float*)d_in[17];
-  const float* si_bn_g= (const float*)d_in[18];
-  const float* si_bn_b= (const float*)d_in[19];
-  const float* si_w2  = (const float*)d_in[20];
-  const float* si_b2  = (const float*)d_in[21];
-  const float* xpw    = (const float*)d_in[22];
-  const float* dt_w   = (const float*)d_in[23];
-  const float* dt_b   = (const float*)d_in[24];
-  const float* Ds     = (const float*)d_in[26];
-
-  float* ws    = (float*)d_ws;
-  float* v_hw  = ws;
-  float* v_wh  = v_hw + 786432;
-  float* xdbl  = v_wh + 786432;
-  float* hend  = xdbl + 1310720;
-  float* Pbuf  = hend + 1572864;
-  float* Hin   = Pbuf + 1572864;
-  float* convx = Hin  + 1572864;
-  float* partial2 = convx + 786432;
-  float* ybuf  = hend;
-  float* att   = xdbl;
-  float* out = (float*)d_out;
-
-  hipLaunchKernelGGL(kQ, dim3(256),  dim3(512), 0, stream, x, qkv_w, v_hw);
-  hipLaunchKernelGGL(kT, dim3(192),  dim3(256), 0, stream, v_hw, v_wh);
-  hipLaunchKernelGGL(kP, dim3(1024), dim3(512), 0, stream, v_hw, v_wh, xpw, xdbl);
-  hipLaunchKernelGGL(kC, dim3(1408), dim3(128), 0, stream, v_hw, v_wh, xdbl, dt_w, dt_b,
-                     dw_w, dw_b, bn1_g, bn1_b, hend, Pbuf, convx, partial2);
-  hipLaunchKernelGGL(kD, dim3(384),  dim3(256), 0, stream, hend, Pbuf, Hin);
-  hipLaunchKernelGGL(kE, dim3(1024), dim3(128), 0, stream, v_hw, v_wh, xdbl, dt_w, dt_b, Hin, ybuf);
-  hipLaunchKernelGGL(kF, dim3(192),  dim3(256), 0, stream, ybuf, v_hw, Ds, att);
-  hipLaunchKernelGGL(kG, dim3(256),  dim3(512), 0, stream, att, convx, partial2,
-                     ci_w1, ci_b1, ci_bn_g, ci_bn_b, ci_w2, ci_b2,
-                     si_w1, si_b1, si_bn_g, si_bn_b, si_w2, si_b2,
-                     proj_w, proj_b, out);
-}
+  float* ws = (float*)d_ws;
+  Params p;
+  p.x      = (const float*)d_in[0];
+  p.qkv_w  = (const float*)d_in[3];
+  p.proj_w = (const float*)d_in[4];
+  p.proj_b = (const float*)d_in[5];
+  p.dw_w   = (const float*)d_in[6];
+  p.dw_b   = (const float*)d_in[7];
+  p.bn_g   = (const float*)d_in[8];
+  p.bn_b   = (const float*)d_in[9];
+  p.ci_w1  = (const float*)d_in[10];
+  p.ci_b1  = (const float*)d_in[11];
+  p.ci_g1  = (const float*)d_in[12];
+  p.ci_bb1 = (const float*)d_in[13];
+  p.ci_w2  = (const float*)d_in[14];
+  p.ci_b2  = (const float*)d_in[15];
+  p.si_w1  = (const float*)d_in[16];
+  p.si_b1  = (const float*)d_in[17];
+  p.si_g1  = (const float*)d_in[18];
+  p.si_bb1 = (const float*)d_in[19];
+  p.si_w2  = (const float*)d_in[20];
+  p.si_b2  = (const float*)d_in[21];
+  p.xpw    = (const float*)d_in[22];
+  p.dt_w   = (const float*)d_in[23];
+  p.dt_b   = (const float*)d_in[24];
+  p.Ds     = (const float*)d_in[26];
+
+  p.vT_hw  = ws;
+  p.vP_hw  = ws + 786432;
+  p.vT_wh  = ws + 1572864;
+  p.xdbl   = ws + 2359296;
+  p.hend   = ws + 3670016;
+  p.Pbuf   = ws + 5242880;
+  p.Hin    = ws + 6815744;
+  p.convxP = ws + 8388608;
+  p.partial= ws + 9175040;
+  p.ybuf   = p.hend;
+  p.out    = (float*)d_out;
+
+  int nb = 0;
+  hipError_t oe = hipOccupancyMaxActiveBlocksPerMultiprocessor(&nb, mega, 256, 0);
+  bool ok = false;
+  if (oe == hipSuccess && nb >= 1){
+    int G = nb * 256;
+    if (G > 512) G = 512;
+    void* args[] = { (void*)&p };
+    ok = (hipLaunchCooperativeKernel(mega, dim3(G), dim3(256), args, 0u, stream) == hipSuccess);
+  }
+  if (!ok){
+    hipLaunchKernelGGL(kP1, dim3(512), dim3(256), 0, stream, p);
+    hipLaunchKernelGGL(kP2, dim3(512), dim3(256), 0, stream, p);
+    hipLaunchKernelGGL(kP3, dim3(512), dim3(256), 0, stream, p);
+    hipLaunchKernelGGL(kP4, dim3(512), dim3(256), 0, stream, p);
+    hipLaunchKernelGGL(kP5, dim3(384), dim3(256), 0, stream, p);
+    hipLaunchKernelGGL(kP6, dim3(512), dim3(256), 0, stream, p);
+    hipLaunchKernelGGL(kP7, dim3(256), dim3(256), 0, stream, p);
+  }
+}
```

Result: slower. 658.6 us (+202.8%).
